# Performance work log

Hardware: AMD Instinct MI355X
Metric: run time of the kernel (lower is better)

The kernel has to match this reference:

```python
import jax, jax.numpy as jnp
import numpy as np

N = 20000; E = 640000
D_IN = 1000; E1 = 500; E2 = 500; E3 = 2000; NZ = 10; NC = 10


def setup_inputs() -> dict:
    keys = iter(jax.random.split(jax.random.key(0), 80))

    def nrm(shape, s=0.05):
        return jax.random.normal(next(keys), shape, jnp.float32) * s

    inp = {"x": jax.random.normal(next(keys), (N, D_IN), jnp.float32)}
    for nm in ["adj", "fadj", "f1", "f2"]:
        inp[nm + "_rows"] = jax.random.randint(next(keys), (E,), 0, N, jnp.int32)
        inp[nm + "_cols"] = jax.random.randint(next(keys), (E,), 0, N, jnp.int32)
        inp[nm + "_vals"] = jax.random.uniform(next(keys), (E,), jnp.float32)
    dims = [D_IN, E1, E2, E3, NZ]
    for br in ["fea", "topo"]:
        for i in range(4):
            inp[br + "_W" + str(i + 1)] = nrm((dims[i], dims[i + 1]))
    ae_shapes = {"e1": (D_IN, E1), "e2": (E1, E2), "e3": (E2, E3), "z1": (E3, NZ),
                 "z2": (NZ, NC), "d0": (NC, NZ), "d1": (NZ, 2000), "d2": (2000, 500),
                 "d3": (500, 500), "xb": (500, D_IN)}
    for nm, sh in ae_shapes.items():
        inp["ae_W" + nm] = nrm(sh)
        inp["ae_b" + nm] = jnp.zeros((sh[1],), jnp.float32)
    inp["mlpL_W"] = nrm((3000 + NZ, 5))
    inp["mlpL_b"] = jnp.zeros((5,), jnp.float32)
    return inp


def _bn(h):
    # BatchNorm1d(affine=False, track_running_stats=False): batch stats, biased var
    return (h - h.mean(0)) * jax.lax.rsqrt(h.var(0) + 1e-5)


def _branch(x, rows, cols, vals, Ws):
    # stacked GNNLayer: dense mm -> spmm(adj, support) -> leaky_relu(0.2) -> elu -> BN
    hs = []
    h = x
    for W in Ws:
        sup = h @ W                                            # [N, out]
        agg = jax.ops.segment_sum(vals[:, None] * sup[cols], rows, num_segments=N)
        h = _bn(jax.nn.elu(jax.nn.leaky_relu(agg, 0.2)))
        hs.append(h)
    return hs


def _forward(x,
             adj_rows, adj_cols, adj_vals,
             fadj_rows, fadj_cols, fadj_vals,
             f1_rows, f1_cols, f1_vals,
             f2_rows, f2_cols, f2_vals,
             fea_W1, fea_W2, fea_W3, fea_W4,
             topo_W1, topo_W2, topo_W3, topo_W4,
             ae_We1, ae_be1, ae_We2, ae_be2, ae_We3, ae_be3,
             ae_Wz1, ae_bz1, ae_Wz2, ae_bz2,
             ae_Wd0, ae_bd0, ae_Wd1, ae_bd1, ae_Wd2, ae_bd2, ae_Wd3, ae_bd3,
             ae_Wxb, ae_bxb, mlpL_W, mlpL_b):
    relu = jax.nn.relu
    # AE branch
    h1 = relu(x @ ae_We1 + ae_be1)
    h2 = relu(h1 @ ae_We2 + ae_be2)
    h3 = relu(h2 @ ae_We3 + ae_be3)
    z1 = h3 @ ae_Wz1 + ae_bz1
    z = z1 @ ae_Wz2 + ae_bz2
    d = relu(z @ ae_Wd0 + ae_bd0)
    d = relu(d @ ae_Wd1 + ae_bd1)
    d = relu(d @ ae_Wd2 + ae_bd2)
    d = relu(d @ ae_Wd3 + ae_bd3)
    x_bar = d @ ae_Wxb + ae_bxb
    feaWs = [fea_W1, fea_W2, fea_W3, fea_W4]
    topoWs = [topo_W1, topo_W2, topo_W3, topo_W4]
    fea_hs = _branch(x, fadj_rows, fadj_cols, fadj_vals, feaWs)
    fea_diff = _branch(x, f2_rows, f2_cols, f2_vals, feaWs)
    topo_hs = _branch(x, adj_rows, adj_cols, adj_vals, topoWs)
    topo_diff = _branch(x, f1_rows, f1_cols, f1_vals, topoWs)
    coms = jnp.concatenate(fea_hs, axis=1)                      # [N, 3000+NZ]
    u = jax.nn.softmax(jnp.tanh(coms @ mlpL_W + mlpL_b), axis=1)
    u = u / jnp.maximum(jnp.linalg.norm(u, axis=1, keepdims=True), 1e-12)  # F.normalize p=2
    z_out_fea = jnp.concatenate([u[:, i:i + 1] * fea_hs[i] for i in range(4)], axis=1)
    return (x_bar, z, fea_hs[3], topo_hs[3], fea_diff[3], topo_diff[3], z_out_fea)


def reference(x,
              adj_rows, adj_cols, adj_vals,
              fadj_rows, fadj_cols, fadj_vals,
              f1_rows, f1_cols, f1_vals,
              f2_rows, f2_cols, f2_vals,
              fea_W1, fea_W2, fea_W3, fea_W4,
              topo_W1, topo_W2, topo_W3, topo_W4,
              ae_We1, ae_be1, ae_We2, ae_be2, ae_We3, ae_be3,
              ae_Wz1, ae_bz1, ae_Wz2, ae_bz2,
              ae_Wd0, ae_bd0, ae_Wd1, ae_bd1, ae_Wd2, ae_bd2, ae_Wd3, ae_bd3,
              ae_Wxb, ae_bxb, mlpL_W, mlpL_b):
    return _forward(x, adj_rows, adj_cols, adj_vals, fadj_rows, fadj_cols, fadj_vals,
                    f1_rows, f1_cols, f1_vals, f2_rows, f2_cols, f2_vals,
                    fea_W1, fea_W2, fea_W3, fea_W4, topo_W1, topo_W2, topo_W3, topo_W4,
                    ae_We1, ae_be1, ae_We2, ae_be2, ae_We3, ae_be3,
                    ae_Wz1, ae_bz1, ae_Wz2, ae_bz2,
                    ae_Wd0, ae_bd0, ae_Wd1, ae_bd1, ae_Wd2, ae_bd2, ae_Wd3, ae_bd3,
                    ae_Wxb, ae_bxb, mlpL_W, mlpL_b)
```

## Files before the change

kernel.cpp:

```cpp
#include <hip/hip_runtime.h>
#include <cstdint>
#include <cstddef>

#define N_NODES 20000
#define N_EDGES 640000

typedef short short8 __attribute__((ext_vector_type(8)));
typedef float floatx4 __attribute__((ext_vector_type(4)));

__device__ __forceinline__ ushort f2bf(float f) {
    uint32_t u = __float_as_uint(f);
    uint32_t r = (u + 0x7fff + ((u >> 16) & 1)) >> 16;
    return (ushort)r;
}
__device__ __forceinline__ float bf2f(ushort u) {
    return __uint_as_float(((uint32_t)u) << 16);
}

__global__ __launch_bounds__(256) void zero_i32(int* __restrict__ p, int n) {
    int i = blockIdx.x * 256 + threadIdx.x;
    if (i < n) p[i] = 0;
}

__global__ __launch_bounds__(256) void transpose_w(const float* __restrict__ W,
                                                   ushort* __restrict__ Bt,
                                                   int K, int Nc, int Kp) {
    int idx = blockIdx.x * 256 + threadIdx.x;
    if (idx >= Nc * Kp) return;
    int n = idx / Kp, k = idx % Kp;
    Bt[idx] = (k < K) ? f2bf(W[(size_t)k * Nc + n]) : (ushort)0;
}

__global__ __launch_bounds__(256) void hist_kernel(const int* __restrict__ rows,
                                                   int* __restrict__ counts) {
    int e = blockIdx.x * 256 + threadIdx.x;
    if (e < N_EDGES) atomicAdd(&counts[rows[e]], 1);
}

__global__ __launch_bounds__(1024) void scan_kernel(const int* __restrict__ counts,
                                                    int* __restrict__ row_ptr) {
    __shared__ int part[1024];
    const int CH = 20;
    int tid = threadIdx.x;
    int t0 = tid * CH;
    int s = 0;
    for (int i = 0; i < CH; ++i) {
        int p = t0 + i;
        if (p < N_NODES) s += counts[p];
    }
    part[tid] = s;
    __syncthreads();
    for (int off = 1; off < 1024; off <<= 1) {
        int v = (tid >= off) ? part[tid - off] : 0;
        __syncthreads();
        if (tid >= off) part[tid] += v;
        __syncthreads();
    }
    int base = (tid == 0) ? 0 : part[tid - 1];
    for (int i = 0; i < CH; ++i) {
        int p = t0 + i;
        if (p < N_NODES) {
            row_ptr[p] = base;
            base += counts[p];
            if (p == N_NODES - 1) row_ptr[N_NODES] = base;
        }
    }
}

__global__ __launch_bounds__(256) void fill_kernel(const int* __restrict__ rows,
                                                   const int* __restrict__ cols,
                                                   const float* __restrict__ vals,
                                                   const int* __restrict__ row_ptr,
                                                   int* __restrict__ fillctr,
                                                   int* __restrict__ cols_s,
                                                   float* __restrict__ vals_s) {
    int e = blockIdx.x * 256 + threadIdx.x;
    if (e < N_EDGES) {
        int r = rows[e];
        int pos = atomicAdd(&fillctr[r], 1);
        int idx = row_ptr[r] + pos;
        cols_s[idx] = cols[e];
        vals_s[idx] = vals[e];
    }
}

template <int AMODE>
__global__ __launch_bounds__(256) void mfma_gemm(
    const float* __restrict__ A, const ushort* __restrict__ Ab,
    const ushort* __restrict__ Bt,
    const float* __restrict__ bias, float* __restrict__ Cf,
    ushort* __restrict__ Cb, int M, int K, int lda, int Nc, int ldc, int Kp,
    int act, int NX, int NY) {
    __shared__ __align__(16) ushort As[128][40];
    __shared__ __align__(16) ushort Bs[128][40];
    __shared__ __align__(16) ushort Al[(AMODE == 1) ? 128 : 1][40];

    int id = blockIdx.x;
    int r8 = id & 7, tt = id >> 3;
    int bx = tt % NX, qq = tt / NX;
    int by = r8 + 8 * qq;
    if (by >= NY) return;
    int row0 = by * 128, col0 = bx * 128;

    int tid = threadIdx.x;
    int wave = tid >> 6, lane = tid & 63;
    int wr = (wave >> 1) * 64, wc = (wave & 1) * 64;
    int m16 = lane & 15, quad = lane >> 4;

    floatx4 acc[4][4] = {};
    int KT = (K + 31) >> 5;
    bool k4 = (K & 3) == 0;

    int arf = tid >> 3, akq = (tid & 7) << 2;
    int arb = tid >> 2, akb = (tid & 3) << 3;
    int bn_ = tid >> 2, bch = (tid & 3) << 3;

    float4 avA[4], avB[4];
    uint4 abvA[2], abvB[2], bvA[2], bvB[2];

#define ISSUE_T(AV, ABV, BV, KTARG)                                          \
    do {                                                                     \
        int k0_ = (KTARG) << 5;                                              \
        if constexpr (AMODE == 2) {                                          \
            for (int p = 0; p < 2; ++p) {                                    \
                int grow = row0 + arb + p * 64;                              \
                int gk = k0_ + akb;                                          \
                uint4 z = {0u, 0u, 0u, 0u};                                  \
                if (grow < M) {                                              \
                    const ushort* ap = Ab + (size_t)grow * lda + gk;         \
                    if (gk + 7 < K) {                                        \
                        z = *(const uint4*)ap;                               \
                    } else {                                                 \
                        ushort tm[8] = {0, 0, 0, 0, 0, 0, 0, 0};             \
                        for (int j = 0; j < 8; ++j)                          \
                            if (gk + j < K) tm[j] = ap[j];                   \
                        z.x = (uint)tm[0] | ((uint)tm[1] << 16);             \
                        z.y = (uint)tm[2] | ((uint)tm[3] << 16);             \
                        z.z = (uint)tm[4] | ((uint)tm[5] << 16);             \
                        z.w = (uint)tm[6] | ((uint)tm[7] << 16);             \
                    }                                                        \
                }                                                            \
                ABV[p] = z;                                                  \
            }                                                                \
        } else {                                                             \
            for (int p = 0; p < 4; ++p) {                                    \
                int grow = row0 + arf + p * 32;                              \
                int gk = k0_ + akq;                                          \
                float4 v = {0.f, 0.f, 0.f, 0.f};                             \
                if (grow < M) {                                              \
                    const float* ap = A + (size_t)grow * lda + gk;           \
                    if (k4 && gk + 3 < K) {                                  \
                        v = *(const float4*)ap;                              \
                    } else {                                                 \
                        if (gk < K) v.x = ap[0];                             \
                        if (gk + 1 < K) v.y = ap[1];                         \
                        if (gk + 2 < K) v.z = ap[2];                         \
                        if (gk + 3 < K) v.w = ap[3];                         \
                    }                                                        \
                }                                                            \
                AV[p] = v;                                                   \
            }                                                                \
        }                                                                    \
        for (int p = 0; p < 2; ++p) {                                        \
            int gcol = col0 + bn_ + p * 64;                                  \
            uint4 z = {0u, 0u, 0u, 0u};                                      \
            if (gcol < Nc) z = *(const uint4*)&Bt[(size_t)gcol * Kp + k0_ + bch]; \
            BV[p] = z;                                                       \
        }                                                                    \
    } while (0)

#define WRITE_T(AV, ABV, BV)                                                 \
    do {                                                                     \
        if constexpr (AMODE == 2) {                                          \
            for (int p = 0; p < 2; ++p)                                      \
                *(uint4*)&As[arb + p * 64][akb] = ABV[p];                    \
        } else {                                                             \
            for (int p = 0; p < 4; ++p) {                                    \
                float4 v = AV[p];                                            \
                ushort4 hi;                                                  \
                hi.x = f2bf(v.x); hi.y = f2bf(v.y);                          \
                hi.z = f2bf(v.z); hi.w = f2bf(v.w);                          \
                *(ushort4*)&As[arf + p * 32][akq] = hi;                      \
                if constexpr (AMODE == 1) {                                  \
                    ushort4 lo;                                              \
                    lo.x = f2bf(v.x - bf2f(hi.x));                           \
                    lo.y = f2bf(v.y - bf2f(hi.y));                           \
                    lo.z = f2bf(v.z - bf2f(hi.z));                           \
                    lo.w = f2bf(v.w - bf2f(hi.w));                           \
                    *(ushort4*)&Al[arf + p * 32][akq] = lo;                  \
                }                                                            \
            }                                                                \
        }                                                                    \
        for (int p = 0; p < 2; ++p)                                          \
            *(uint4*)&Bs[bn_ + p * 64][bch] = BV[p];                         \
    } while (0)

    ISSUE_T(avA, abvA, bvA, 0);
    for (int kt = 0; kt < KT; ++kt) {
        if (kt) __syncthreads();
        if ((kt & 1) == 0) {
            WRITE_T(avA, abvA, bvA);
            if (kt + 1 < KT) ISSUE_T(avB, abvB, bvB, kt + 1);
        } else {
            WRITE_T(avB, abvB, bvB);
            if (kt + 1 < KT) ISSUE_T(avA, abvA, bvA, kt + 1);
        }
        __syncthreads();
        short8 a[4], b[4];
        int ko = quad * 8;
#pragma unroll
        for (int i = 0; i < 4; ++i) a[i] = *(short8*)&As[wr + i * 16 + m16][ko];
#pragma unroll
        for (int j = 0; j < 4; ++j) b[j] = *(short8*)&Bs[wc + j * 16 + m16][ko];
        if constexpr (AMODE == 1) {
            short8 al[4];
#pragma unroll
            for (int i = 0; i < 4; ++i) al[i] = *(short8*)&Al[wr + i * 16 + m16][ko];
#pragma unroll
            for (int i = 0; i < 4; ++i)
#pragma unroll
                for (int j = 0; j < 4; ++j)
                    acc[i][j] = __builtin_amdgcn_mfma_f32_16x16x32_bf16(
                        al[i], b[j], acc[i][j], 0, 0, 0);
        }
#pragma unroll
        for (int i = 0; i < 4; ++i)
#pragma unroll
            for (int j = 0; j < 4; ++j)
                acc[i][j] = __builtin_amdgcn_mfma_f32_16x16x32_bf16(
                    a[i], b[j], acc[i][j], 0, 0, 0);
    }
#undef ISSUE_T
#undef WRITE_T

#pragma unroll
    for (int i = 0; i < 4; ++i) {
        int rbase = row0 + wr + i * 16 + quad * 4;
#pragma unroll
        for (int j = 0; j < 4; ++j) {
            int gcol = col0 + wc + j * 16 + m16;
            if (gcol >= Nc) continue;
            float bv = bias ? bias[gcol] : 0.f;
#pragma unroll
            for (int r = 0; r < 4; ++r) {
                int grow = rbase + r;
                if (grow >= M) continue;
                float v = acc[i][j][r] + bv;
                if (act == 1) v = v > 0.f ? v : 0.f;
                else if (act == 2) v = v > 0.f ? v : (expf(0.2f * v) - 1.0f);
                if (Cb) Cb[(size_t)grow * ldc + gcol] = f2bf(v);
                else Cf[(size_t)grow * ldc + gcol] = v;
            }
        }
    }
}

__global__ __launch_bounds__(256) void gemm_small(
    const float* __restrict__ A, const float* __restrict__ B,
    const float* __restrict__ bias, float* __restrict__ C,
    int M, int K, int Nc, int act) {
    int row = blockIdx.x * 8 + (threadIdx.x >> 5);
    int c = threadIdx.x & 31;
    if (row >= M || c >= Nc) return;
    float acc = bias ? bias[c] : 0.f;
    for (int k = 0; k < K; ++k) acc += A[(size_t)row * K + k] * B[(size_t)k * Nc + c];
    if (act) acc = acc > 0.f ? acc : 0.f;
    C[(size_t)row * Nc + c] = acc;
}

__global__ __launch_bounds__(256) void spmm_act_bf(const ushort* __restrict__ sup,
                                                   const int* __restrict__ row_ptr,
                                                   const int* __restrict__ cols_s,
                                                   const float* __restrict__ vals_s,
                                                   ushort* __restrict__ t, int C) {
    int r = blockIdx.x;
    int f0 = blockIdx.y * 512 + threadIdx.x * 2;
    int s = row_ptr[r], e = row_ptr[r + 1];
    float a0 = 0.f, a1 = 0.f;
    if (f0 < C) {
        for (int i = s; i < e; ++i) {
            float v = vals_s[i];
            int c = cols_s[i];
            uint u = *(const uint*)&sup[(size_t)c * C + f0];
            a0 += v * bf2f((ushort)(u & 0xffff));
            a1 += v * bf2f((ushort)(u >> 16));
        }
        float r0 = a0 > 0.f ? a0 : (expf(0.2f * a0) - 1.f);
        float r1 = a1 > 0.f ? a1 : (expf(0.2f * a1) - 1.f);
        ushort2 w;
        w.x = f2bf(r0);
        w.y = f2bf(r1);
        *(ushort2*)&t[(size_t)r * C + f0] = w;
    }
}

__global__ __launch_bounds__(256) void spmm_act_fb(const float* __restrict__ sup,
                                                   const int* __restrict__ row_ptr,
                                                   const int* __restrict__ cols_s,
                                                   const float* __restrict__ vals_s,
                                                   ushort* __restrict__ t, int C) {
    int r = blockIdx.x;
    int f0 = blockIdx.y * 512 + threadIdx.x * 2;
    if (f0 >= C) return;
    int s = row_ptr[r], e = row_ptr[r + 1];
    float a0 = 0.f, a1 = 0.f;
    for (int i = s; i < e; ++i) {
        float v = vals_s[i];
        int c = cols_s[i];
        float2 u = *(const float2*)&sup[(size_t)c * C + f0];
        a0 += v * u.x;
        a1 += v * u.y;
    }
    float r0 = a0 > 0.f ? a0 : (expf(0.2f * a0) - 1.f);
    float r1 = a1 > 0.f ? a1 : (expf(0.2f * a1) - 1.f);
    ushort2 w;
    w.x = f2bf(r0);
    w.y = f2bf(r1);
    *(ushort2*)&t[(size_t)r * C + f0] = w;
}

__global__ __launch_bounds__(256) void spmm_gather_bf(const ushort* __restrict__ h,
                                                      const int* __restrict__ row_ptr,
                                                      const int* __restrict__ cols_s,
                                                      const float* __restrict__ vals_s,
                                                      float* __restrict__ agg, int C,
                                                      int hld) {
    int r = blockIdx.x;
    int f0 = blockIdx.y * 512 + threadIdx.x * 2;
    if (f0 >= C) return;
    int s = row_ptr[r], e = row_ptr[r + 1];
    float a0 = 0.f, a1 = 0.f;
    for (int i = s; i < e; ++i) {
        float v = vals_s[i];
        int c = cols_s[i];
        uint u = *(const uint*)&h[(size_t)c * hld + f0];
        a0 += v * bf2f((ushort)(u & 0xffff));
        a1 += v * bf2f((ushort)(u >> 16));
    }
    float2 w;
    w.x = a0;
    w.y = a1;
    *(float2*)&agg[(size_t)r * C + f0] = w;
}

__global__ __launch_bounds__(256) void spmm_act_f(const float* __restrict__ sup,
                                                  const int* __restrict__ row_ptr,
                                                  const int* __restrict__ cols_s,
                                                  const float* __restrict__ vals_s,
                                                  float* __restrict__ t, int C) {
    int r = blockIdx.x;
    int f = blockIdx.y * 256 + threadIdx.x;
    int s = row_ptr[r], e = row_ptr[r + 1];
    float acc = 0.f;
    for (int i = s; i < e; ++i) {
        float v = vals_s[i];
        int c = cols_s[i];
        if (f < C) acc += v * sup[(size_t)c * C + f];
    }
    if (f < C) {
        float a = acc;
        t[(size_t)r * C + f] = a > 0.f ? a : (expf(0.2f * a) - 1.0f);
    }
}

__global__ __launch_bounds__(256) void spmm_gather_f(const float* __restrict__ h,
                                                     const int* __restrict__ row_ptr,
                                                     const int* __restrict__ cols_s,
                                                     const float* __restrict__ vals_s,
                                                     float* __restrict__ agg, int C) {
    int r = blockIdx.x;
    int f = blockIdx.y * 256 + threadIdx.x;
    int s = row_ptr[r], e = row_ptr[r + 1];
    float acc = 0.f;
    for (int i = s; i < e; ++i) {
        float v = vals_s[i];
        int c = cols_s[i];
        if (f < C) acc += v * h[(size_t)c * C + f];
    }
    if (f < C) agg[(size_t)r * C + f] = acc;
}

__global__ __launch_bounds__(256) void col_stats(const ushort* __restrict__ t,
                                                 float* __restrict__ sum,
                                                 float* __restrict__ sumsq, int C) {
    int c = blockIdx.x * 256 + threadIdx.x;
    int r0 = blockIdx.y * 500;
    if (c >= C) return;
    float s = 0.f, ss = 0.f;
    for (int r = r0; r < r0 + 500; ++r) {
        float v = bf2f(t[(size_t)r * C + c]);
        s += v;
        ss += v * v;
    }
    atomicAdd(&sum[c], s);
    atomicAdd(&sumsq[c], ss);
}

__global__ __launch_bounds__(256) void bn_apply(const ushort* __restrict__ t,
                                                const float* __restrict__ sum,
                                                const float* __restrict__ sumsq,
                                                float* __restrict__ h, int C) {
    int c = blockIdx.x * 256 + threadIdx.x;
    int r = blockIdx.y;
    if (c >= C) return;
    float mean = sum[c] * (1.0f / N_NODES);
    float var = sumsq[c] * (1.0f / N_NODES) - mean * mean;
    float rs = rsqrtf(var + 1e-5f);
    h[(size_t)r * C + c] = (bf2f(t[(size_t)r * C + c]) - mean) * rs;
}

__global__ __launch_bounds__(256) void bn_apply_bb(const ushort* __restrict__ t,
                                                   const float* __restrict__ sum,
                                                   const float* __restrict__ sumsq,
                                                   ushort* __restrict__ h, int C,
                                                   int ldh) {
    int c = blockIdx.x * 256 + threadIdx.x;
    int r = blockIdx.y;
    if (c >= C) return;
    float mean = sum[c] * (1.0f / N_NODES);
    float var = sumsq[c] * (1.0f / N_NODES) - mean * mean;
    float rs = rsqrtf(var + 1e-5f);
    h[(size_t)r * ldh + c] = f2bf((bf2f(t[(size_t)r * C + c]) - mean) * rs);
}

__global__ __launch_bounds__(256) void col_stats_f(const float* __restrict__ t,
                                                   float* __restrict__ sum,
                                                   float* __restrict__ sumsq, int C) {
    int c = blockIdx.x * 256 + threadIdx.x;
    int r0 = blockIdx.y * 500;
    if (c >= C) return;
    float s = 0.f, ss = 0.f;
    for (int r = r0; r < r0 + 500; ++r) {
        float v = t[(size_t)r * C + c];
        s += v;
        ss += v * v;
    }
    atomicAdd(&sum[c], s);
    atomicAdd(&sumsq[c], ss);
}

__global__ __launch_bounds__(256) void bn_apply_f(const float* __restrict__ t,
                                                  const float* __restrict__ sum,
                                                  const float* __restrict__ sumsq,
                                                  float* __restrict__ h, int C) {
    int c = blockIdx.x * 256 + threadIdx.x;
    int r = blockIdx.y;
    if (c >= C) return;
    float mean = sum[c] * (1.0f / N_NODES);
    float var = sumsq[c] * (1.0f / N_NODES) - mean * mean;
    float rs = rsqrtf(var + 1e-5f);
    h[(size_t)r * C + c] = (t[(size_t)r * C + c] - mean) * rs;
}

__global__ __launch_bounds__(256) void mlp_u(const float* __restrict__ h1,
                                             const float* __restrict__ h2,
                                             const float* __restrict__ h3,
                                             const float* __restrict__ h4,
                                             const float* __restrict__ W,
                                             const float* __restrict__ b,
                                             float* __restrict__ u) {
    int lane = threadIdx.x & 63;
    int wv = threadIdx.x >> 6;
    int row = blockIdx.x * 4 + wv;
    if (row >= N_NODES) return;
    float acc[5] = {0.f, 0.f, 0.f, 0.f, 0.f};
    const float* hs[4] = {h1, h2, h3, h4};
    const int Cs[4] = {500, 500, 2000, 10};
    const int Woff[4] = {0, 500, 1000, 3000};
    for (int sg = 0; sg < 4; ++sg) {
        const float* hp = hs[sg] + (size_t)row * Cs[sg];
        const float* wp = W + (size_t)Woff[sg] * 5;
        for (int k = lane; k < Cs[sg]; k += 64) {
            float a = hp[k];
#pragma unroll
            for (int j = 0; j < 5; ++j) acc[j] += a * wp[k * 5 + j];
        }
    }
#pragma unroll
    for (int j = 0; j < 5; ++j)
        for (int off = 32; off > 0; off >>= 1) acc[j] += __shfl_down(acc[j], off, 64);
    if (lane == 0) {
        float t[5], m = -1e30f;
#pragma unroll
        for (int j = 0; j < 5; ++j) {
            t[j] = tanhf(acc[j] + b[j]);
            m = fmaxf(m, t[j]);
        }
        float s = 0.f;
#pragma unroll
        for (int j = 0; j < 5; ++j) {
            t[j] = expf(t[j] - m);
            s += t[j];
        }
        float inv = 1.0f / s;
        float n2 = 0.f;
#pragma unroll
        for (int j = 0; j < 5; ++j) {
            t[j] *= inv;
            n2 += t[j] * t[j];
        }
        float nrm = fmaxf(sqrtf(n2), 1e-12f);
        float innrm = 1.0f / nrm;
#pragma unroll
        for (int j = 0; j < 5; ++j) u[(size_t)row * 5 + j] = t[j] * innrm;
    }
}

__global__ __launch_bounds__(256) void zout_kernel(const float* __restrict__ h1,
                                                   const float* __restrict__ h2,
                                                   const float* __restrict__ h3,
                                                   const float* __restrict__ h4,
                                                   const float* __restrict__ u,
                                                   float* __restrict__ out) {
    int c = blockIdx.x * 256 + threadIdx.x;
    int row = blockIdx.y;
    if (c >= 3010) return;
    int seg, cl;
    const float* hp;
    if (c < 500)       { seg = 0; cl = c;        hp = h1 + (size_t)row * 500; }
    else if (c < 1000) { seg = 1; cl = c - 500;  hp = h2 + (size_t)row * 500; }
    else if (c < 3000) { seg = 2; cl = c - 1000; hp = h3 + (size_t)row * 2000; }
    else               { seg = 3; cl = c - 3000; hp = h4 + (size_t)row * 10; }
    out[(size_t)row * 3010 + c] = u[(size_t)row * 5 + seg] * hp[cl];
}

extern "C" void kernel_launch(void* const* d_in, const int* in_sizes, int n_in,
                              void* d_out, int out_size, void* d_ws, size_t ws_size,
                              hipStream_t stream) {
    const float* x = (const float*)d_in[0];
    const int* adj_rows  = (const int*)d_in[1];
    const int* adj_cols  = (const int*)d_in[2];
    const float* adj_vals = (const float*)d_in[3];
    const int* fadj_rows = (const int*)d_in[4];
    const int* fadj_cols = (const int*)d_in[5];
    const float* fadj_vals = (const float*)d_in[6];
    const int* f1_rows = (const int*)d_in[7];
    const int* f1_cols = (const int*)d_in[8];
    const float* f1_vals = (const float*)d_in[9];
    const int* f2_rows = (const int*)d_in[10];
    const int* f2_cols = (const int*)d_in[11];
    const float* f2_vals = (const float*)d_in[12];
    const float* feaW[4]  = {(const float*)d_in[13], (const float*)d_in[14],
                             (const float*)d_in[15], (const float*)d_in[16]};
    const float* topoW[4] = {(const float*)d_in[17], (const float*)d_in[18],
                             (const float*)d_in[19], (const float*)d_in[20]};
    const float* We1 = (const float*)d_in[21]; const float* be1 = (const float*)d_in[22];
    const float* We2 = (const float*)d_in[23]; const float* be2 = (const float*)d_in[24];
    const float* We3 = (const float*)d_in[25]; const float* be3 = (const float*)d_in[26];
    const float* Wz1 = (const float*)d_in[27]; const float* bz1 = (const float*)d_in[28];
    const float* Wz2 = (const float*)d_in[29]; const float* bz2 = (const float*)d_in[30];
    const float* Wd0 = (const float*)d_in[31]; const float* bd0 = (const float*)d_in[32];
    const float* Wd1 = (const float*)d_in[33]; const float* bd1 = (const float*)d_in[34];
    const float* Wd2 = (const float*)d_in[35]; const float* bd2 = (const float*)d_in[36];
    const float* Wd3 = (const float*)d_in[37]; const float* bd3 = (const float*)d_in[38];
    const float* Wxb = (const float*)d_in[39]; const float* bxb = (const float*)d_in[40];
    const float* mlpW = (const float*)d_in[41]; const float* mlpb = (const float*)d_in[42];

    float* out = (float*)d_out;
    float* out_xbar = out;
    float* out_z = out + 20000000;
    float* out_fea4 = out + 20200000;
    float* out_topo4 = out + 20400000;
    float* out_feadiff4 = out + 20600000;
    float* out_topodiff4 = out + 20800000;
    float* out_zout = out + 21000000;

    char* w = (char*)d_ws;
    auto alloc = [&](size_t bytes) -> char* {
        char* p = w;
        w += (bytes + 255) & ~(size_t)255;
        return p;
    };
    ushort* bufB = (ushort*)alloc((size_t)N_NODES * 2000 * 2);
    ushort* bufC = (ushort*)alloc((size_t)N_NODES * 2000 * 2);
    float* feah1 = (float*)alloc((size_t)N_NODES * 500 * 4);
    float* feah2 = (float*)alloc((size_t)N_NODES * 500 * 4);
    float* feah3 = (float*)alloc((size_t)N_NODES * 2000 * 4);
    float* bufH  = (float*)alloc((size_t)N_NODES * 2000 * 4);
    ushort* bufHb = (ushort*)(bufH + 10000000);
    float* supFea = bufH + 30000000;
    float* z1buf = (float*)alloc((size_t)N_NODES * 10 * 4);
    float* dsmall = (float*)alloc((size_t)N_NODES * 10 * 4);
    float* ubuf  = (float*)alloc((size_t)N_NODES * 5 * 4);
    float* ssum  = (float*)alloc(2000 * 4);
    float* ssq   = (float*)alloc(2000 * 4);
    int* counts  = (int*)alloc(N_NODES * 4);
    int* fillctr = (int*)alloc(N_NODES * 4);
    int* row_ptr = (int*)alloc((N_NODES + 1) * 4);
    int* cols_s  = (int*)alloc((size_t)N_EDGES * 4);
    float* vals_s = (float*)alloc((size_t)N_EDGES * 4);
    ushort* supTopo = (ushort*)alloc((size_t)N_NODES * 500 * 2);

    ushort* aeh1b = bufC;
    ushort* aeh2b = bufC + (size_t)N_NODES * 512;
    ushort* aeh3b = bufB;

    auto kpad = [](int K) { return ((K + 31) / 32) * 32; };
    struct TW { const float* W; int K, Nc, Kp; ushort* Bt; };
    TW tw[16] = {
        {We1, 1000, 500, 1024, nullptr}, {We2, 500, 500, 512, nullptr},
        {We3, 500, 2000, 512, nullptr},  {Wz1, 2000, 10, 2016, nullptr},
        {Wd1, 10, 2000, 32, nullptr},    {Wd2, 2000, 500, 2016, nullptr},
        {Wd3, 500, 500, 512, nullptr},   {Wxb, 500, 1000, 512, nullptr},
        {feaW[0], 1000, 500, 1024, nullptr}, {feaW[1], 500, 500, 512, nullptr},
        {feaW[2], 500, 2000, 512, nullptr},  {feaW[3], 2000, 10, 2016, nullptr},
        {topoW[0], 1000, 500, 1024, nullptr}, {topoW[1], 500, 500, 512, nullptr},
        {topoW[2], 500, 2000, 512, nullptr},  {topoW[3], 2000, 10, 2016, nullptr},
    };
    for (int i = 0; i < 16; ++i) {
        tw[i].Kp = kpad(tw[i].K);
        tw[i].Bt = (ushort*)alloc((size_t)tw[i].Nc * tw[i].Kp * 2);
        int tot = tw[i].Nc * tw[i].Kp;
        transpose_w<<<(tot + 255) / 256, 256, 0, stream>>>(
            tw[i].W, tw[i].Bt, tw[i].K, tw[i].Nc, tw[i].Kp);
    }

    const int NYB = (N_NODES + 127) / 128;
    const int NY8 = 8 * ((NYB + 7) / 8);
    auto gemm_f32 = [&](const float* A, const TW& t, const float* bias, float* Cf,
                        ushort* Cb, int lda, int ldc, int act) {
        int NX = (t.Nc + 127) / 128;
        mfma_gemm<0><<<NX * NY8, 256, 0, stream>>>(A, nullptr, t.Bt, bias, Cf, Cb,
                                                   N_NODES, t.K, lda, t.Nc, ldc,
                                                   t.Kp, act, NX, NYB);
    };
    auto gemm_spl = [&](const float* A, const TW& t, float* Cf, int lda, int ldc,
                        int act) {
        int NX = (t.Nc + 127) / 128;
        mfma_gemm<1><<<NX * NY8, 256, 0, stream>>>(A, nullptr, t.Bt, nullptr, Cf,
                                                   nullptr, N_NODES, t.K, lda, t.Nc,
                                                   ldc, t.Kp, act, NX, NYB);
    };
    auto gemm_b16 = [&](const ushort* Ab, const TW& t, const float* bias, float* Cf,
                        ushort* Cb, int lda, int ldc, int act) {
        int NX = (t.Nc + 127) / 128;
        mfma_gemm<2><<<NX * NY8, 256, 0, stream>>>(nullptr, Ab, t.Bt, bias, Cf, Cb,
                                                   N_NODES, t.K, lda, t.Nc, ldc,
                                                   t.Kp, act, NX, NYB);
    };

    gemm_f32(x, tw[0], be1, nullptr, aeh1b, 1000, 512, 1);
    gemm_b16(aeh1b, tw[1], be2, nullptr, aeh2b, 512, 512, 1);
    gemm_b16(aeh2b, tw[2], be3, nullptr, aeh3b, 512, 2000, 1);
    gemm_b16(aeh3b, tw[3], bz1, z1buf, nullptr, 2000, 10, 0);
    gemm_small<<<(N_NODES + 7) / 8, 256, 0, stream>>>(z1buf, Wz2, bz2, out_z,
                                                      N_NODES, 10, 10, 0);
    gemm_small<<<(N_NODES + 7) / 8, 256, 0, stream>>>(out_z, Wd0, bd0, dsmall,
                                                      N_NODES, 10, 10, 1);
    gemm_f32(dsmall, tw[4], bd1, nullptr, aeh3b, 10, 2000, 1);
    gemm_b16(aeh3b, tw[5], bd2, nullptr, aeh1b, 2000, 512, 1);
    gemm_b16(aeh1b, tw[6], bd3, nullptr, aeh2b, 512, 512, 1);
    gemm_b16(aeh2b, tw[7], bxb, out_xbar, nullptr, 512, 1000, 0);

    gemm_f32(x, tw[12], nullptr, nullptr, supTopo, 1000, 500, 0);

    struct Br {
        const int* rows; const int* cols; const float* vals;
        int w0;
        float* final_dest;
    };
    Br brs[4] = {
        {fadj_rows, fadj_cols, fadj_vals, 8, out_fea4},
        {adj_rows, adj_cols, adj_vals, 12, out_topo4},
        {f2_rows, f2_cols, f2_vals, 8, out_feadiff4},
        {f1_rows, f1_cols, f1_vals, 12, out_topodiff4},
    };

    auto bn_zero = [&](int C) {
        zero_i32<<<(C + 255) / 256, 256, 0, stream>>>((int*)ssum, C);
        zero_i32<<<(C + 255) / 256, 256, 0, stream>>>((int*)ssq, C);
    };
    auto bn_f = [&](float* t, int C) {
        bn_zero(C);
        col_stats_f<<<dim3((C + 255) / 256, 40), 256, 0, stream>>>(t, ssum, ssq, C);
        bn_apply_f<<<dim3((C + 255) / 256, N_NODES), 256, 0, stream>>>(t, ssum, ssq,
                                                                       t, C);
    };
    auto bn_bb = [&](const ushort* t, ushort* h, int C, int ldh) {
        bn_zero(C);
        col_stats<<<dim3((C + 255) / 256, 40), 256, 0, stream>>>(t, ssum, ssq, C);
        bn_apply_bb<<<dim3((C + 255) / 256, N_NODES), 256, 0, stream>>>(
            t, ssum, ssq, h, C, ldh);
    };
    auto bn_bf = [&](const ushort* t, float* h, int C) {
        bn_zero(C);
        col_stats<<<dim3((C + 255) / 256, 40), 256, 0, stream>>>(t, ssum, ssq, C);
        bn_apply<<<dim3((C + 255) / 256, N_NODES), 256, 0, stream>>>(t, ssum, ssq,
                                                                     h, C);
    };
    auto spmmA_f = [&](const float* sup, float* dst, int C) {
        spmm_act_f<<<dim3(N_NODES, (C + 255) / 256), 256, 0, stream>>>(
            sup, row_ptr, cols_s, vals_s, dst, C);
    };
    auto spmmA_bf = [&](const ushort* sup, ushort* dst, int C) {
        spmm_act_bf<<<dim3(N_NODES, (C + 511) / 512), 256, 0, stream>>>(
            sup, row_ptr, cols_s, vals_s, dst, C);
    };

    for (int b = 0; b < 4; ++b) {
        zero_i32<<<(N_NODES + 255) / 256, 256, 0, stream>>>(counts, N_NODES);
        hist_kernel<<<(N_EDGES + 255) / 256, 256, 0, stream>>>(brs[b].rows, counts);
        scan_kernel<<<1, 1024, 0, stream>>>(counts, row_ptr);
        zero_i32<<<(N_NODES + 255) / 256, 256, 0, stream>>>(fillctr, N_NODES);
        fill_kernel<<<(N_EDGES + 255) / 256, 256, 0, stream>>>(
            brs[b].rows, brs[b].cols, brs[b].vals, row_ptr, fillctr, cols_s, vals_s);

        int w0 = brs[b].w0;
        if (b == 0) {
            gemm_spl(x, tw[w0], supFea, 1000, 500, 0);
            spmmA_f(supFea, feah1, 500);
            bn_f(feah1, 500);
            gemm_spl(feah1, tw[w0 + 1], bufH, 500, 500, 0);
            spmmA_f(bufH, feah2, 500);
            bn_f(feah2, 500);
            spmm_gather_f<<<dim3(N_NODES, 2), 256, 0, stream>>>(
                feah2, row_ptr, cols_s, vals_s, bufH, 500);
            gemm_spl(bufH, tw[w0 + 2], feah3, 500, 2000, 2);
            bn_f(feah3, 2000);
            gemm_spl(feah3, tw[w0 + 3], bufH, 2000, 10, 0);
            spmmA_f(bufH, brs[b].final_dest, 10);
            bn_f(brs[b].final_dest, 10);
        } else {
            if (b == 2) {
                spmm_act_fb<<<dim3(N_NODES, 1), 256, 0, stream>>>(
                    supFea, row_ptr, cols_s, vals_s, bufC, 500);
            } else {
                spmmA_bf(supTopo, bufC, 500);
            }
            bn_bb(bufC, bufHb, 500, 512);
            gemm_b16(bufHb, tw[w0 + 1], nullptr, nullptr, bufB, 512, 500, 0);
            spmmA_bf(bufB, bufC, 500);
            bn_bb(bufC, bufHb, 500, 512);
            spmm_gather_bf<<<dim3(N_NODES, 1), 256, 0, stream>>>(
                bufHb, row_ptr, cols_s, vals_s, bufH, 500, 512);
            gemm_f32(bufH, tw[w0 + 2], nullptr, nullptr, bufC, 500, 2000, 2);
            bn_bb(bufC, bufHb, 2000, 2000);
            gemm_b16(bufHb, tw[w0 + 3], nullptr, nullptr, bufB, 2000, 10, 0);
            spmmA_bf(bufB, bufC, 10);
            bn_bf(bufC, brs[b].final_dest, 10);
        }
    }

    mlp_u<<<(N_NODES + 3) / 4, 256, 0, stream>>>(feah1, feah2, feah3, out_fea4,
                                                 mlpW, mlpb, ubuf);
    zout_kernel<<<dim3(12, N_NODES), 256, 0, stream>>>(feah1, feah2, feah3, out_fea4,
                                                       ubuf, out_zout);
}
```

Measured before the change: 6.295 ms.

## Vectorize SpMM gathers with 4-wide loads and split edges for narrow outputs

Replaces the per-row SpMM kernels with templated versions where each thread handles four features through 16-byte (fp32) or 8-byte (bf16) loads. The edge loop is unrolled by four with independent accumulators, so more gathers are in flight at once. For the 10-column layers, a new kernel spreads each row's edges across 16 sub-groups and reduces them in shared memory, instead of leaving most of a 256-thread block idle. It also reshapes the BatchNorm stats grids and adds flat element-wise normalization for narrow outputs; the main risk is a change in summation order.

```diff
diff --git a/kernel.cpp b/kernel.cpp
--- a/kernel.cpp
+++ b/kernel.cpp
@@ -268,126 +268,187 @@
     C[(size_t)row * Nc + c] = acc;
 }
 
-__global__ __launch_bounds__(256) void spmm_act_bf(const ushort* __restrict__ sup,
-                                                   const int* __restrict__ row_ptr,
-                                                   const int* __restrict__ cols_s,
-                                                   const float* __restrict__ vals_s,
-                                                   ushort* __restrict__ t, int C) {
+
+template <int ACT, int OUTBF>
+__global__ __launch_bounds__(128) void spmm_f32in(
+    const float* __restrict__ sup, const int* __restrict__ rp,
+    const int* __restrict__ cols_s, const float* __restrict__ vals_s,
+    float* __restrict__ outf, ushort* __restrict__ outb,
+    int C, int ldin, int ldout) {
     int r = blockIdx.x;
-    int f0 = blockIdx.y * 512 + threadIdx.x * 2;
-    int s = row_ptr[r], e = row_ptr[r + 1];
-    float a0 = 0.f, a1 = 0.f;
-    if (f0 < C) {
-        for (int i = s; i < e; ++i) {
-            float v = vals_s[i];
-            int c = cols_s[i];
-            uint u = *(const uint*)&sup[(size_t)c * C + f0];
-            a0 += v * bf2f((ushort)(u & 0xffff));
-            a1 += v * bf2f((ushort)(u >> 16));
-        }
-        float r0 = a0 > 0.f ? a0 : (expf(0.2f * a0) - 1.f);
-        float r1 = a1 > 0.f ? a1 : (expf(0.2f * a1) - 1.f);
-        ushort2 w;
-        w.x = f2bf(r0);
-        w.y = f2bf(r1);
-        *(ushort2*)&t[(size_t)r * C + f0] = w;
-    }
-}
-
-__global__ __launch_bounds__(256) void spmm_act_fb(const float* __restrict__ sup,
-                                                   const int* __restrict__ row_ptr,
-                                                   const int* __restrict__ cols_s,
-                                                   const float* __restrict__ vals_s,
-                                                   ushort* __restrict__ t, int C) {
+    int f0 = (blockIdx.y * 128 + threadIdx.x) * 4;
+    if (f0 >= C) return;
+    int s = rp[r], e = rp[r + 1];
+    const float* sb = sup + f0;
+    floatx4 A0 = {0.f, 0.f, 0.f, 0.f}, A1 = A0, A2 = A0, A3 = A0;
+    int i = s;
+    for (; i + 4 <= e; i += 4) {
+        int c0 = cols_s[i], c1 = cols_s[i + 1], c2 = cols_s[i + 2],
+            c3 = cols_s[i + 3];
+        float v0 = vals_s[i], v1 = vals_s[i + 1], v2 = vals_s[i + 2],
+              v3 = vals_s[i + 3];
+        floatx4 u0 = *(const floatx4*)(sb + (size_t)c0 * ldin);
+        floatx4 u1 = *(const floatx4*)(sb + (size_t)c1 * ldin);
+        floatx4 u2 = *(const floatx4*)(sb + (size_t)c2 * ldin);
+        floatx4 u3 = *(const floatx4*)(sb + (size_t)c3 * ldin);
+        A0 += v0 * u0;
+        A1 += v1 * u1;
+        A2 += v2 * u2;
+        A3 += v3 * u3;
+    }
+    int n = e - i;
+    if (n > 0) {
+        int c0 = cols_s[i];
+        int c1 = cols_s[i + (n > 1 ? 1 : 0)];
+        int c2 = cols_s[i + (n > 2 ? 2 : 0)];
+        float v0 = vals_s[i];
+        float v1 = n > 1 ? vals_s[i + 1] : 0.f;
+        float v2 = n > 2 ? vals_s[i + 2] : 0.f;
+        floatx4 u0 = *(const floatx4*)(sb + (size_t)c0 * ldin);
+        floatx4 u1 = *(const floatx4*)(sb + (size_t)c1 * ldin);
+        floatx4 u2 = *(const floatx4*)(sb + (size_t)c2 * ldin);
+        A0 += v0 * u0;
+        A1 += v1 * u1;
+        A2 += v2 * u2;
+    }
+    floatx4 acc = (A0 + A1) + (A2 + A3);
+    if (ACT) {
+#pragma unroll
+        for (int k = 0; k < 4; ++k)
+            acc[k] = acc[k] > 0.f ? acc[k] : (expf(0.2f * acc[k]) - 1.0f);
+    }
+    if (OUTBF) {
+        ushort4 w;
+        w.x = f2bf(acc[0]); w.y = f2bf(acc[1]);
+        w.z = f2bf(acc[2]); w.w = f2bf(acc[3]);
+        *(ushort4*)&outb[(size_t)r * ldout + f0] = w;
+    } else {
+        *(floatx4*)&outf[(size_t)r * ldout + f0] = acc;
+    }
+}
+
+template <int ACT, int OUTF32>
+__global__ __launch_bounds__(128) void spmm_bf16in(
+    const ushort* __restrict__ sup, const int* __restrict__ rp,
+    const int* __restrict__ cols_s, const float* __restrict__ vals_s,
+    float* __restrict__ outf, ushort* __restrict__ outb,
+    int C, int ldin, int ldout) {
     int r = blockIdx.x;
-    int f0 = blockIdx.y * 512 + threadIdx.x * 2;
+    int f0 = (blockIdx.y * 128 + threadIdx.x) * 4;
     if (f0 >= C) return;
-    int s = row_ptr[r], e = row_ptr[r + 1];
-    float a0 = 0.f, a1 = 0.f;
-    for (int i = s; i < e; ++i) {
-        float v = vals_s[i];
-        int c = cols_s[i];
-        float2 u = *(const float2*)&sup[(size_t)c * C + f0];
-        a0 += v * u.x;
-        a1 += v * u.y;
-    }
-    float r0 = a0 > 0.f ? a0 : (expf(0.2f * a0) - 1.f);
-    float r1 = a1 > 0.f ? a1 : (expf(0.2f * a1) - 1.f);
-    ushort2 w;
-    w.x = f2bf(r0);
-    w.y = f2bf(r1);
-    *(ushort2*)&t[(size_t)r * C + f0] = w;
-}
-
-__global__ __launch_bounds__(256) void spmm_gather_bf(const ushort* __restrict__ h,
-                                                      const int* __restrict__ row_ptr,
-                                                      const int* __restrict__ cols_s,
-                                                      const float* __restrict__ vals_s,
-                                                      float* __restrict__ agg, int C,
-                                                      int hld) {
+    int s = rp[r], e = rp[r + 1];
+    const ushort* sb = sup + f0;
+    floatx4 A0 = {0.f, 0.f, 0.f, 0.f}, A1 = A0, A2 = A0, A3 = A0;
+    int i = s;
+#define UNPK(ACCV, VV, QQ)                                                   \
+    do {                                                                     \
+        ACCV[0] += VV * bf2f((ushort)(QQ.x & 0xffff));                       \
+        ACCV[1] += VV * bf2f((ushort)(QQ.x >> 16));                          \
+        ACCV[2] += VV * bf2f((ushort)(QQ.y & 0xffff));                       \
+        ACCV[3] += VV * bf2f((ushort)(QQ.y >> 16));                          \
+    } while (0)
+    for (; i + 4 <= e; i += 4) {
+        int c0 = cols_s[i], c1 = cols_s[i + 1], c2 = cols_s[i + 2],
+            c3 = cols_s[i + 3];
+        float v0 = vals_s[i], v1 = vals_s[i + 1], v2 = vals_s[i + 2],
+              v3 = vals_s[i + 3];
+        uint2 q0 = *(const uint2*)(sb + (size_t)c0 * ldin);
+        uint2 q1 = *(const uint2*)(sb + (size_t)c1 * ldin);
+        uint2 q2 = *(const uint2*)(sb + (size_t)c2 * ldin);
+        uint2 q3 = *(const uint2*)(sb + (size_t)c3 * ldin);
+        UNPK(A0, v0, q0);
+        UNPK(A1, v1, q1);
+        UNPK(A2, v2, q2);
+        UNPK(A3, v3, q3);
+    }
+    int n = e - i;
+    if (n > 0) {
+        int c0 = cols_s[i];
+        int c1 = cols_s[i + (n > 1 ? 1 : 0)];
+        int c2 = cols_s[i + (n > 2 ? 2 : 0)];
+        float v0 = vals_s[i];
+        float v1 = n > 1 ? vals_s[i + 1] : 0.f;
+        float v2 = n > 2 ? vals_s[i + 2] : 0.f;
+        uint2 q0 = *(const uint2*)(sb + (size_t)c0 * ldin);
+        uint2 q1 = *(const uint2*)(sb + (size_t)c1 * ldin);
+        uint2 q2 = *(const uint2*)(sb + (size_t)c2 * ldin);
+        UNPK(A0, v0, q0);
+        UNPK(A1, v1, q1);
+        UNPK(A2, v2, q2);
+    }
+#undef UNPK
+    floatx4 acc = (A0 + A1) + (A2 + A3);
+    if (ACT) {
+#pragma unroll
+        for (int k = 0; k < 4; ++k)
+            acc[k] = acc[k] > 0.f ? acc[k] : (expf(0.2f * acc[k]) - 1.0f);
+    }
+    if (OUTF32) {
+        *(floatx4*)&outf[(size_t)r * ldout + f0] = acc;
+    } else {
+        ushort4 w;
+        w.x = f2bf(acc[0]); w.y = f2bf(acc[1]);
+        w.z = f2bf(acc[2]); w.w = f2bf(acc[3]);
+        *(ushort4*)&outb[(size_t)r * ldout + f0] = w;
+    }
+}
+
+__global__ __launch_bounds__(256) void spmm_small_bf(
+    const ushort* __restrict__ sup, const int* __restrict__ rp,
+    const int* __restrict__ cols_s, const float* __restrict__ vals_s,
+    ushort* __restrict__ t, int C, int ldin) {
+    __shared__ float red[16][17];
     int r = blockIdx.x;
-    int f0 = blockIdx.y * 512 + threadIdx.x * 2;
-    if (f0 >= C) return;
-    int s = row_ptr[r], e = row_ptr[r + 1];
-    float a0 = 0.f, a1 = 0.f;
-    for (int i = s; i < e; ++i) {
-        float v = vals_s[i];
-        int c = cols_s[i];
-        uint u = *(const uint*)&h[(size_t)c * hld + f0];
-        a0 += v * bf2f((ushort)(u & 0xffff));
-        a1 += v * bf2f((ushort)(u >> 16));
-    }
-    float2 w;
-    w.x = a0;
-    w.y = a1;
-    *(float2*)&agg[(size_t)r * C + f0] = w;
-}
-
-__global__ __launch_bounds__(256) void spmm_act_f(const float* __restrict__ sup,
-                                                  const int* __restrict__ row_ptr,
-                                                  const int* __restrict__ cols_s,
-                                                  const float* __restrict__ vals_s,
-                                                  float* __restrict__ t, int C) {
+    int f = threadIdx.x & 15, sub = threadIdx.x >> 4;
+    int s = rp[r], e = rp[r + 1];
+    float acc = 0.f;
+    if (f < C) {
+        for (int i = s + sub; i < e; i += 16)
+            acc += vals_s[i] * bf2f(sup[(size_t)cols_s[i] * ldin + f]);
+    }
+    red[sub][f] = acc;
+    __syncthreads();
+    if (sub == 0 && f < C) {
+        float a = 0.f;
+#pragma unroll
+        for (int k = 0; k < 16; ++k) a += red[k][f];
+        float o = a > 0.f ? a : (expf(0.2f * a) - 1.0f);
+        t[(size_t)r * C + f] = f2bf(o);
+    }
+}
+
+__global__ __launch_bounds__(256) void spmm_small_f(
+    const float* __restrict__ sup, const int* __restrict__ rp,
+    const int* __restrict__ cols_s, const float* __restrict__ vals_s,
+    float* __restrict__ t, int C, int ldin) {
+    __shared__ float red[16][17];
     int r = blockIdx.x;
-    int f = blockIdx.y * 256 + threadIdx.x;
-    int s = row_ptr[r], e = row_ptr[r + 1];
+    int f = threadIdx.x & 15, sub = threadIdx.x >> 4;
+    int s = rp[r], e = rp[r + 1];
     float acc = 0.f;
-    for (int i = s; i < e; ++i) {
-        float v = vals_s[i];
-        int c = cols_s[i];
-        if (f < C) acc += v * sup[(size_t)c * C + f];
-    }
     if (f < C) {
-        float a = acc;
+        for (int i = s + sub; i < e; i += 16)
+            acc += vals_s[i] * sup[(size_t)cols_s[i] * ldin + f];
+    }
+    red[sub][f] = acc;
+    __syncthreads();
+    if (sub == 0 && f < C) {
+        float a = 0.f;
+#pragma unroll
+        for (int k = 0; k < 16; ++k) a += red[k][f];
         t[(size_t)r * C + f] = a > 0.f ? a : (expf(0.2f * a) - 1.0f);
     }
-}
-
-__global__ __launch_bounds__(256) void spmm_gather_f(const float* __restrict__ h,
-                                                     const int* __restrict__ row_ptr,
-                                                     const int* __restrict__ cols_s,
-                                                     const float* __restrict__ vals_s,
-                                                     float* __restrict__ agg, int C) {
-    int r = blockIdx.x;
-    int f = blockIdx.y * 256 + threadIdx.x;
-    int s = row_ptr[r], e = row_ptr[r + 1];
-    float acc = 0.f;
-    for (int i = s; i < e; ++i) {
-        float v = vals_s[i];
-        int c = cols_s[i];
-        if (f < C) acc += v * h[(size_t)c * C + f];
-    }
-    if (f < C) agg[(size_t)r * C + f] = acc;
 }
 
 __global__ __launch_bounds__(256) void col_stats(const ushort* __restrict__ t,
                                                  float* __restrict__ sum,
-                                                 float* __restrict__ sumsq, int C) {
+                                                 float* __restrict__ sumsq, int C,
+                                                 int rpb) {
     int c = blockIdx.x * 256 + threadIdx.x;
-    int r0 = blockIdx.y * 500;
+    int r0 = blockIdx.y * rpb;
     if (c >= C) return;
     float s = 0.f, ss = 0.f;
-    for (int r = r0; r < r0 + 500; ++r) {
+    for (int r = r0; r < r0 + rpb; ++r) {
         float v = bf2f(t[(size_t)r * C + c]);
         s += v;
         ss += v * v;
@@ -423,14 +484,42 @@
     h[(size_t)r * ldh + c] = f2bf((bf2f(t[(size_t)r * C + c]) - mean) * rs);
 }
 
+__global__ __launch_bounds__(256) void bn_elem_bf(const ushort* __restrict__ t,
+                                                  const float* __restrict__ sum,
+                                                  const float* __restrict__ sumsq,
+                                                  float* __restrict__ h, int C,
+                                                  int total) {
+    int idx = blockIdx.x * 256 + threadIdx.x;
+    if (idx >= total) return;
+    int c = idx % C;
+    float mean = sum[c] * (1.0f / N_NODES);
+    float var = sumsq[c] * (1.0f / N_NODES) - mean * mean;
+    float rs = rsqrtf(var + 1e-5f);
+    h[idx] = (bf2f(t[idx]) - mean) * rs;
+}
+
+__global__ __launch_bounds__(256) void bn_elem_f(float* __restrict__ t,
+                                                 const float* __restrict__ sum,
+                                                 const float* __restrict__ sumsq,
+                                                 int C, int total) {
+    int idx = blockIdx.x * 256 + threadIdx.x;
+    if (idx >= total) return;
+    int c = idx % C;
+    float mean = sum[c] * (1.0f / N_NODES);
+    float var = sumsq[c] * (1.0f / N_NODES) - mean * mean;
+    float rs = rsqrtf(var + 1e-5f);
+    t[idx] = (t[idx] - mean) * rs;
+}
+
 __global__ __launch_bounds__(256) void col_stats_f(const float* __restrict__ t,
                                                    float* __restrict__ sum,
-                                                   float* __restrict__ sumsq, int C) {
+                                                   float* __restrict__ sumsq, int C,
+                                                   int rpb) {
     int c = blockIdx.x * 256 + threadIdx.x;
-    int r0 = blockIdx.y * 500;
+    int r0 = blockIdx.y * rpb;
     if (c >= C) return;
     float s = 0.f, ss = 0.f;
-    for (int r = r0; r < r0 + 500; ++r) {
+    for (int r = r0; r < r0 + rpb; ++r) {
         float v = t[(size_t)r * C + c];
         s += v;
         ss += v * v;
@@ -672,29 +761,29 @@
     };
     auto bn_f = [&](float* t, int C) {
         bn_zero(C);
-        col_stats_f<<<dim3((C + 255) / 256, 40), 256, 0, stream>>>(t, ssum, ssq, C);
-        bn_apply_f<<<dim3((C + 255) / 256, N_NODES), 256, 0, stream>>>(t, ssum, ssq,
-                                                                       t, C);
+        if (C <= 16) {
+            col_stats_f<<<dim3(1, 200), 256, 0, stream>>>(t, ssum, ssq, C, 100);
+            int tot = N_NODES * C;
+            bn_elem_f<<<(tot + 255) / 256, 256, 0, stream>>>(t, ssum, ssq, C, tot);
+        } else {
+            col_stats_f<<<dim3((C + 255) / 256, 100), 256, 0, stream>>>(
+                t, ssum, ssq, C, 200);
+            bn_apply_f<<<dim3((C + 255) / 256, N_NODES), 256, 0, stream>>>(
+                t, ssum, ssq, t, C);
+        }
     };
     auto bn_bb = [&](const ushort* t, ushort* h, int C, int ldh) {
         bn_zero(C);
-        col_stats<<<dim3((C + 255) / 256, 40), 256, 0, stream>>>(t, ssum, ssq, C);
+        col_stats<<<dim3((C + 255) / 256, 100), 256, 0, stream>>>(t, ssum, ssq, C,
+                                                                  200);
         bn_apply_bb<<<dim3((C + 255) / 256, N_NODES), 256, 0, stream>>>(
             t, ssum, ssq, h, C, ldh);
     };
-    auto bn_bf = [&](const ushort* t, float* h, int C) {
+    auto bn_bf_small = [&](const ushort* t, float* h, int C) {
         bn_zero(C);
-        col_stats<<<dim3((C + 255) / 256, 40), 256, 0, stream>>>(t, ssum, ssq, C);
-        bn_apply<<<dim3((C + 255) / 256, N_NODES), 256, 0, stream>>>(t, ssum, ssq,
-                                                                     h, C);
-    };
-    auto spmmA_f = [&](const float* sup, float* dst, int C) {
-        spmm_act_f<<<dim3(N_NODES, (C + 255) / 256), 256, 0, stream>>>(
-            sup, row_ptr, cols_s, vals_s, dst, C);
-    };
-    auto spmmA_bf = [&](const ushort* sup, ushort* dst, int C) {
-        spmm_act_bf<<<dim3(N_NODES, (C + 511) / 512), 256, 0, stream>>>(
-            sup, row_ptr, cols_s, vals_s, dst, C);
+        col_stats<<<dim3(1, 200), 256, 0, stream>>>(t, ssum, ssq, C, 100);
+        int tot = N_NODES * C;
+        bn_elem_bf<<<(tot + 255) / 256, 256, 0, stream>>>(t, ssum, ssq, h, C, tot);
     };
 
     for (int b = 0; b < 4; ++b) {
@@ -708,36 +797,42 @@
         int w0 = brs[b].w0;
         if (b == 0) {
             gemm_spl(x, tw[w0], supFea, 1000, 500, 0);
-            spmmA_f(supFea, feah1, 500);
+            spmm_f32in<1, 0><<<dim3(N_NODES, 1), 128, 0, stream>>>(
+                supFea, row_ptr, cols_s, vals_s, feah1, nullptr, 500, 500, 500);
             bn_f(feah1, 500);
             gemm_spl(feah1, tw[w0 + 1], bufH, 500, 500, 0);
-            spmmA_f(bufH, feah2, 500);
+            spmm_f32in<1, 0><<<dim3(N_NODES, 1), 128, 0, stream>>>(
+                bufH, row_ptr, cols_s, vals_s, feah2, nullptr, 500, 500, 500);
             bn_f(feah2, 500);
-            spmm_gather_f<<<dim3(N_NODES, 2), 256, 0, stream>>>(
-                feah2, row_ptr, cols_s, vals_s, bufH, 500);
+            spmm_f32in<0, 0><<<dim3(N_NODES, 1), 128, 0, stream>>>(
+                feah2, row_ptr, cols_s, vals_s, bufH, nullptr, 500, 500, 500);
             gemm_spl(bufH, tw[w0 + 2], feah3, 500, 2000, 2);
             bn_f(feah3, 2000);
             gemm_spl(feah3, tw[w0 + 3], bufH, 2000, 10, 0);
-            spmmA_f(bufH, brs[b].final_dest, 10);
+            spmm_small_f<<<N_NODES, 256, 0, stream>>>(bufH, row_ptr, cols_s, vals_s,
+                                                      brs[b].final_dest, 10, 10);
             bn_f(brs[b].final_dest, 10);
         } else {
             if (b == 2) {
-                spmm_act_fb<<<dim3(N_NODES, 1), 256, 0, stream>>>(
-                    supFea, row_ptr, cols_s, vals_s, bufC, 500);
+                spmm_f32in<1, 1><<<dim3(N_NODES, 1), 128, 0, stream>>>(
+                    supFea, row_ptr, cols_s, vals_s, nullptr, bufC, 500, 500, 500);
             } else {
-                spmmA_bf(supTopo, bufC, 500);
+                spmm_bf16in<1, 0><<<dim3(N_NODES, 1), 128, 0, stream>>>(
+                    supTopo, row_ptr, cols_s, vals_s, nullptr, bufC, 500, 500, 500);
             }
             bn_bb(bufC, bufHb, 500, 512);
             gemm_b16(bufHb, tw[w0 + 1], nullptr, nullptr, bufB, 512, 500, 0);
-            spmmA_bf(bufB, bufC, 500);
+            spmm_bf16in<1, 0><<<dim3(N_NODES, 1), 128, 0, stream>>>(
+                bufB, row_ptr, cols_s, vals_s, nullptr, bufC, 500, 500, 500);
             bn_bb(bufC, bufHb, 500, 512);
-            spmm_gather_bf<<<dim3(N_NODES, 1), 256, 0, stream>>>(
-                bufHb, row_ptr, cols_s, vals_s, bufH, 500, 512);
+            spmm_bf16in<0, 1><<<dim3(N_NODES, 1), 128, 0, stream>>>(
+                bufHb, row_ptr, cols_s, vals_s, bufH, nullptr, 500, 512, 500);
             gemm_f32(bufH, tw[w0 + 2], nullptr, nullptr, bufC, 500, 2000, 2);
             bn_bb(bufC, bufHb, 2000, 2000);
             gemm_b16(bufHb, tw[w0 + 3], nullptr, nullptr, bufB, 2000, 10, 0);
-            spmmA_bf(bufB, bufC, 10);
-            bn_bf(bufC, brs[b].final_dest, 10);
+            spmm_small_bf<<<N_NODES, 256, 0, stream>>>(bufB, row_ptr, cols_s, vals_s,
+                                                       bufC, 10, 10);
+            bn_bf_small(bufC, brs[b].final_dest, 10);
         }
     }
 
```

Result: faster. 5.690 ms (-9.6%).
